# Performance work log

Hardware: AMD Instinct MI355X
Metric: run time of the kernel (lower is better)

Reference implementation:

```python
import jax, jax.numpy as jnp
import numpy as np

N = 100000      # nodes
E = 500000      # edges
NODE_IN = 60
EDGE_IN = 8
H = 256         # hidden
L = 8           # GINEConv layers
G = 64          # graphs in batch
BN_EPS = 1e-5


def setup_inputs() -> dict:
    key = jax.random.key(0)
    ks = jax.random.split(key, 40)
    s = 0.05
    f32 = jnp.float32
    inp = {
        "x": jax.random.normal(ks[0], (N, NODE_IN), f32),
        "edge_index": jax.random.randint(ks[1], (2, E), 0, N),
        "edge_attr": jax.random.normal(ks[2], (E, EDGE_IN), f32),
        "batch": jnp.sort(jax.random.randint(ks[3], (N,), 0, G)),
        # x_proj: Linear(node_in->H) + BatchNorm1d (eval-mode running stats)
        "xproj_W": jax.random.normal(ks[4], (NODE_IN, H), f32) * s,
        "xproj_b": jnp.zeros((H,), f32),
        "xp_gamma": jnp.ones((H,), f32),
        "xp_beta": jnp.zeros((H,), f32),
        "xp_mean": jax.random.normal(ks[5], (H,), f32) * 0.01,
        "xp_var": jax.random.uniform(ks[6], (H,), f32, 0.5, 1.5),
        # stacked GINEConv params (L layers)
        "edge_W": jax.random.normal(ks[7], (L, EDGE_IN, H), f32) * s,
        "edge_b": jnp.zeros((L, H), f32),
        "mlp_W1": jax.random.normal(ks[8], (L, H, H), f32) * s,
        "mlp_b1": jnp.zeros((L, H), f32),
        "mlp_W2": jax.random.normal(ks[9], (L, H, H), f32) * s,
        "mlp_b2": jnp.zeros((L, H), f32),
        "eps": jnp.zeros((L,), f32),  # GINE eps (default 0, not trained)
        # per-layer BatchNorm (eval-mode)
        "bn_gamma": jnp.ones((L, H), f32),
        "bn_beta": jnp.zeros((L, H), f32),
        "bn_mean": jax.random.normal(ks[10], (L, H), f32) * 0.01,
        "bn_var": jax.random.uniform(ks[11], (L, H), f32, 0.5, 1.5),
        # head: Linear(H->H/2) ReLU Dropout Linear(H/2->1)
        "head_W1": jax.random.normal(ks[12], (H, H // 2), f32) * s,
        "head_b1": jnp.zeros((H // 2,), f32),
        "head_W2": jax.random.normal(ks[13], (H // 2, 1), f32) * s,
        "head_b2": jnp.zeros((1,), f32),
    }
    return inp


def _bn(x, gamma, beta, mean, var):
    # eval-mode BatchNorm1d with running stats
    return (x - mean) * (gamma * jax.lax.rsqrt(var + BN_EPS)) + beta


def reference(x, edge_index, edge_attr, batch,
              xproj_W, xproj_b, xp_gamma, xp_beta, xp_mean, xp_var,
              edge_W, edge_b, mlp_W1, mlp_b1, mlp_W2, mlp_b2, eps,
              bn_gamma, bn_beta, bn_mean, bn_var,
              head_W1, head_b1, head_W2, head_b2):
    src, dst = edge_index[0], edge_index[1]  # source -> target aggregation
    # x_proj: Linear + BN + ReLU
    h = jax.nn.relu(_bn(x @ xproj_W + xproj_b, xp_gamma, xp_beta, xp_mean, xp_var))
    for l in range(L):
        # GINEConv: msg = ReLU(x_j + lin(edge_attr)); sum-aggregate at target
        e = edge_attr @ edge_W[l] + edge_b[l]                 # [E,H]
        m = jax.nn.relu(h[src] + e)                           # [E,H] gather + add
        agg = jax.ops.segment_sum(m, dst, num_segments=N)     # [N,H] scatter-add
        z = (1.0 + eps[l]) * h + agg
        z = jax.nn.relu(z @ mlp_W1[l] + mlp_b1[l]) @ mlp_W2[l] + mlp_b2[l]
        # BN + ReLU (dropout is identity in eval)
        h = jax.nn.relu(_bn(z, bn_gamma[l], bn_beta[l], bn_mean[l], bn_var[l]))
    # global_mean_pool over batch ids
    gsum = jax.ops.segment_sum(h, batch, num_segments=G)      # [G,H]
    cnt = jax.ops.segment_sum(jnp.ones((N, 1), h.dtype), batch, num_segments=G)
    g = gsum / jnp.maximum(cnt, 1.0)
    # head MLP -> scalar per graph
    hid = jax.nn.relu(g @ head_W1 + head_b1)
    out = (hid @ head_W2 + head_b2)[:, 0]                     # [G]
    return out
```

## Files before the change

kernel.cpp:

```cpp
#include <hip/hip_runtime.h>

#define N_NODES 100000
#define N_EDGES 500000
#define NODE_IN 60
#define EDGE_IN 8
#define HID 256
#define NLAYERS 8
#define NGRAPH 64
#define BN_EPS 1e-5f
#define SY_PITCH 520

typedef __attribute__((ext_vector_type(4))) float f32x4;
typedef __attribute__((ext_vector_type(4))) short short4v;
typedef __attribute__((ext_vector_type(8))) short short8v;
typedef __attribute__((ext_vector_type(4))) unsigned short u16x4;
typedef unsigned short u16;

__device__ __forceinline__ u16 f2bf(float f) {
    unsigned int u = __builtin_bit_cast(unsigned int, f);
    u += 0x7fffu + ((u >> 16) & 1u);
    return (u16)(u >> 16);
}
__device__ __forceinline__ float bf2f(u16 u) {
    unsigned int x = ((unsigned int)u) << 16;
    return __builtin_bit_cast(float, x);
}
__device__ __forceinline__ float lo_f(unsigned int d) {
    return __builtin_bit_cast(float, d << 16);
}
__device__ __forceinline__ float hi_f(unsigned int d) {
    return __builtin_bit_cast(float, d & 0xffff0000u);
}

__device__ __forceinline__ void g2lds16(const void* g, void* l) {
    __builtin_amdgcn_global_load_lds(
        (const __attribute__((address_space(1))) void*)g,
        (__attribute__((address_space(3))) void*)l, 16, 0, 0);
}

template<int KT, bool WITH_BN>
__global__ __launch_bounds__(256, 2)
void mfma_gemm(const u16* A, const u16* Bt,
               const float* __restrict__ bias,
               const float* __restrict__ gamma, const float* __restrict__ beta,
               const float* __restrict__ mean,  const float* __restrict__ var,
               u16* Cout, int M)
{
    __shared__ u16 smem[24576];
    u16* sA = smem;
    u16* sB = smem + 8192;

    const int tid  = threadIdx.x;
    const int lane = tid & 63;
    const int wv   = tid >> 6;
    const int lrow = lane & 15;
    const int g    = lane >> 4;
    const int m0   = blockIdx.x * 128;
    const int ldab = KT * 128;
    const int lsub = lane >> 3;
    const int gsw  = ((lane & 7) * 16) ^ (lsub << 4);

    f32x4 acc[8][4] = {};

    for (int kt = 0; kt < KT; ++kt) {
        #pragma unroll
        for (int i = 0; i < 4; ++i) {
            const int row = i * 32 + wv * 8 + lsub;
            g2lds16((const char*)A + (size_t)(m0 + row) * ldab + kt * 128 + gsw,
                    (char*)sA + i * 4096 + wv * 1024);
        }
        #pragma unroll
        for (int i = 0; i < 8; ++i) {
            const int row = i * 32 + wv * 8 + lsub;
            g2lds16((const char*)Bt + (size_t)row * ldab + kt * 128 + gsw,
                    (char*)sB + i * 4096 + wv * 1024);
        }
        __syncthreads();

        #pragma unroll
        for (int ks = 0; ks < 2; ++ks) {
            const int off1 = ks * 64 + 8 * g;
            const int off2 = off1 + 32;
            short8v bfrag[4];
            #pragma unroll
            for (int nb = 0; nb < 4; ++nb) {
                const int col = wv * 64 + nb * 16 + lrow;
                const int sw  = (col & 7) << 4;
                short4v lo = *(const short4v*)((const char*)sB + col * 128 + (off1 ^ sw));
                short4v hi = *(const short4v*)((const char*)sB + col * 128 + (off2 ^ sw));
                short8v b;
                b[0] = lo[0]; b[1] = lo[1]; b[2] = lo[2]; b[3] = lo[3];
                b[4] = hi[0]; b[5] = hi[1]; b[6] = hi[2]; b[7] = hi[3];
                bfrag[nb] = b;
            }
            #pragma unroll
            for (int mb = 0; mb < 8; ++mb) {
                const int row = mb * 16 + lrow;
                const int sw  = (row & 7) << 4;
                short4v lo = *(const short4v*)((const char*)sA + row * 128 + (off1 ^ sw));
                short4v hi = *(const short4v*)((const char*)sA + row * 128 + (off2 ^ sw));
                short8v a;
                a[0] = lo[0]; a[1] = lo[1]; a[2] = lo[2]; a[3] = lo[3];
                a[4] = hi[0]; a[5] = hi[1]; a[6] = hi[2]; a[7] = hi[3];
                #pragma unroll
                for (int nb = 0; nb < 4; ++nb)
                    acc[mb][nb] = __builtin_amdgcn_mfma_f32_16x16x32_bf16(a, bfrag[nb], acc[mb][nb], 0, 0, 0);
            }
        }
        __syncthreads();
    }

    #pragma unroll
    for (int mb = 0; mb < 8; ++mb) {
        #pragma unroll
        for (int r = 0; r < 4; ++r) {
            const int row = m0 + mb * 16 + g * 4 + r;
            if (row >= M) continue;
            #pragma unroll
            for (int nb = 0; nb < 4; ++nb) {
                const int col = wv * 64 + nb * 16 + lrow;
                float v = acc[mb][nb][r] + bias[col];
                if constexpr (WITH_BN)
                    v = (v - mean[col]) * (gamma[col] * rsqrtf(var[col] + BN_EPS)) + beta[col];
                v = fmaxf(v, 0.f);
                Cout[(size_t)row * HID + col] = f2bf(v);
            }
        }
    }
}

__global__ __launch_bounds__(256, 2)
void fused_mlp(const u16* __restrict__ Z, const u16* __restrict__ W1t,
               const u16* __restrict__ W2t,
               const float* __restrict__ b1,
               const float* __restrict__ scale2, const float* __restrict__ shift2,
               u16* __restrict__ Hout, int M)
{
    __shared__ u16 smem[37120];
    u16* sA = smem;
    u16* sB = sA + 4096;
    u16* sY = sB + 16384;

    const int tid  = threadIdx.x;
    const int lane = tid & 63;
    const int wv   = tid >> 6;
    const int lrow = lane & 15;
    const int g    = lane >> 4;
    const int m0   = blockIdx.x * 64;
    const int lsub = lane >> 3;
    const int gsw  = ((lane & 7) * 16) ^ (lsub << 4);

    f32x4 acc[4][4] = {};

    for (int kt = 0; kt < 4; ++kt) {
        #pragma unroll
        for (int i = 0; i < 2; ++i) {
            const int row = i * 32 + wv * 8 + lsub;
            g2lds16((const char*)Z + (size_t)(m0 + row) * 512 + kt * 128 + gsw,
                    (char*)sA + i * 4096 + wv * 1024);
        }
        #pragma unroll
        for (int i = 0; i < 8; ++i) {
            const int row = i * 32 + wv * 8 + lsub;
            g2lds16((const char*)W1t + (size_t)row * 512 + kt * 128 + gsw,
                    (char*)sB + i * 4096 + wv * 1024);
        }
        __syncthreads();

        #pragma unroll
        for (int ks = 0; ks < 2; ++ks) {
            const int off1 = ks * 64 + 8 * g;
            const int off2 = off1 + 32;
            short8v bfrag[4];
            #pragma unroll
            for (int nb = 0; nb < 4; ++nb) {
                const int col = wv * 64 + nb * 16 + lrow;
                const int sw  = (col & 7) << 4;
                short4v lo = *(const short4v*)((const char*)sB + col * 128 + (off1 ^ sw));
                short4v hi = *(const short4v*)((const char*)sB + col * 128 + (off2 ^ sw));
                short8v b;
                b[0] = lo[0]; b[1] = lo[1]; b[2] = lo[2]; b[3] = lo[3];
                b[4] = hi[0]; b[5] = hi[1]; b[6] = hi[2]; b[7] = hi[3];
                bfrag[nb] = b;
            }
            #pragma unroll
            for (int mb = 0; mb < 4; ++mb) {
                const int row = mb * 16 + lrow;
                const int sw  = (row & 7) << 4;
                short4v lo = *(const short4v*)((const char*)sA + row * 128 + (off1 ^ sw));
                short4v hi = *(const short4v*)((const char*)sA + row * 128 + (off2 ^ sw));
                short8v a;
                a[0] = lo[0]; a[1] = lo[1]; a[2] = lo[2]; a[3] = lo[3];
                a[4] = hi[0]; a[5] = hi[1]; a[6] = hi[2]; a[7] = hi[3];
                #pragma unroll
                for (int nb = 0; nb < 4; ++nb)
                    acc[mb][nb] = __builtin_amdgcn_mfma_f32_16x16x32_bf16(a, bfrag[nb], acc[mb][nb], 0, 0, 0);
            }
        }
        __syncthreads();
    }

    float b1v[4];
    #pragma unroll
    for (int nb = 0; nb < 4; ++nb) b1v[nb] = b1[wv * 64 + nb * 16 + lrow];
    #pragma unroll
    for (int mb = 0; mb < 4; ++mb) {
        #pragma unroll
        for (int r = 0; r < 4; ++r) {
            const int row = mb * 16 + g * 4 + r;
            #pragma unroll
            for (int nb = 0; nb < 4; ++nb) {
                const int col = wv * 64 + nb * 16 + lrow;
                const float v = fmaxf(acc[mb][nb][r] + b1v[nb], 0.f);
                *(u16*)((char*)sY + row * SY_PITCH + col * 2) = f2bf(v);
            }
        }
    }
    __syncthreads();

    f32x4 acc2[4][4] = {};
    for (int kt2 = 0; kt2 < 4; ++kt2) {
        #pragma unroll
        for (int i = 0; i < 8; ++i) {
            const int row = i * 32 + wv * 8 + lsub;
            g2lds16((const char*)W2t + (size_t)row * 512 + kt2 * 128 + gsw,
                    (char*)sB + i * 4096 + wv * 1024);
        }
        __syncthreads();

        #pragma unroll
        for (int ks = 0; ks < 2; ++ks) {
            const int off1 = ks * 64 + 8 * g;
            const int off2 = off1 + 32;
            const int yo1  = kt2 * 128 + off1;
            const int yo2  = yo1 + 32;
            short8v bfrag[4];
            #pragma unroll
            for (int nb = 0; nb < 4; ++nb) {
                const int col = wv * 64 + nb * 16 + lrow;
                const int sw  = (col & 7) << 4;
                short4v lo = *(const short4v*)((const char*)sB + col * 128 + (off1 ^ sw));
                short4v hi = *(const short4v*)((const char*)sB + col * 128 + (off2 ^ sw));
                short8v b;
                b[0] = lo[0]; b[1] = lo[1]; b[2] = lo[2]; b[3] = lo[3];
                b[4] = hi[0]; b[5] = hi[1]; b[6] = hi[2]; b[7] = hi[3];
                bfrag[nb] = b;
            }
            #pragma unroll
            for (int mb = 0; mb < 4; ++mb) {
                const int row = mb * 16 + lrow;
                short4v lo = *(const short4v*)((const char*)sY + row * SY_PITCH + yo1);
                short4v hi = *(const short4v*)((const char*)sY + row * SY_PITCH + yo2);
                short8v a;
                a[0] = lo[0]; a[1] = lo[1]; a[2] = lo[2]; a[3] = lo[3];
                a[4] = hi[0]; a[5] = hi[1]; a[6] = hi[2]; a[7] = hi[3];
                #pragma unroll
                for (int nb = 0; nb < 4; ++nb)
                    acc2[mb][nb] = __builtin_amdgcn_mfma_f32_16x16x32_bf16(a, bfrag[nb], acc2[mb][nb], 0, 0, 0);
            }
        }
        __syncthreads();
    }

    float scl[4], shf[4];
    #pragma unroll
    for (int nb = 0; nb < 4; ++nb) {
        const int col = wv * 64 + nb * 16 + lrow;
        scl[nb] = scale2[col];
        shf[nb] = shift2[col];
    }
    #pragma unroll
    for (int mb = 0; mb < 4; ++mb) {
        #pragma unroll
        for (int r = 0; r < 4; ++r) {
            const int row = m0 + mb * 16 + g * 4 + r;
            if (row >= M) continue;
            #pragma unroll
            for (int nb = 0; nb < 4; ++nb) {
                const int col = wv * 64 + nb * 16 + lrow;
                const float v = fmaxf(acc2[mb][nb][r] * scl[nb] + shf[nb], 0.f);
                Hout[(size_t)row * HID + col] = f2bf(v);
            }
        }
    }
}

__global__ __launch_bounds__(256)
void convw_kernel(const float* __restrict__ W, u16* __restrict__ Wt)
{
    size_t i = (size_t)blockIdx.x * 256 + threadIdx.x;
    const int mat = (int)(i >> 16);
    const int idx = (int)(i & 65535);
    const int n = idx >> 8, k = idx & 255;
    Wt[i] = f2bf(W[(size_t)mat * 65536 + (size_t)k * 256 + n]);
}

__global__ __launch_bounds__(256)
void convwx_kernel(const float* __restrict__ W, u16* __restrict__ Wt)
{
    int i = blockIdx.x * 256 + threadIdx.x;
    const int n = i >> 6, k = i & 63;
    Wt[i] = (k < NODE_IN) ? f2bf(W[(size_t)k * HID + n]) : (u16)0;
}

__global__ __launch_bounds__(256)
void convx_kernel(const float* __restrict__ x, u16* __restrict__ xbf)
{
    size_t i = (size_t)blockIdx.x * 256 + threadIdx.x;
    if (i >= (size_t)N_NODES * 64) return;
    const int n = (int)(i >> 6), k = (int)(i & 63);
    xbf[i] = (k < NODE_IN) ? f2bf(x[(size_t)n * NODE_IN + k]) : (u16)0;
}

__global__ __launch_bounds__(256)
void bnfold_kernel(const float* __restrict__ b2, const float* __restrict__ gamma,
                   const float* __restrict__ beta, const float* __restrict__ mean,
                   const float* __restrict__ var,
                   float* __restrict__ scale, float* __restrict__ shift)
{
    int i = blockIdx.x * 256 + threadIdx.x;
    if (i >= NLAYERS * HID) return;
    const float s = gamma[i] * rsqrtf(var[i] + BN_EPS);
    scale[i] = s;
    shift[i] = (b2[i] - mean[i]) * s + beta[i];
}

__global__ __launch_bounds__(256)
void deg_count_kernel(const int* __restrict__ dst, int* __restrict__ deg, int E)
{
    int e = blockIdx.x * 256 + threadIdx.x;
    if (e < E) atomicAdd(&deg[dst[e]], 1);
}

__global__ __launch_bounds__(256)
void scan1_kernel(const int* __restrict__ deg, int* __restrict__ rowptr,
                  int* __restrict__ bsum, int n)
{
    __shared__ int s[256];
    const int tid = threadIdx.x;
    const int i = blockIdx.x * 256 + tid;
    const int v = (i < n) ? deg[i] : 0;
    s[tid] = v;
    __syncthreads();
    #pragma unroll
    for (int d = 1; d < 256; d <<= 1) {
        int t = (tid >= d) ? s[tid - d] : 0;
        __syncthreads();
        s[tid] += t;
        __syncthreads();
    }
    if (i < n) rowptr[i] = s[tid] - v;
    if (tid == 255) bsum[blockIdx.x] = s[255];
}

__global__ void scan2_kernel(int* bsum, int nb, int* rowptr, int n)
{
    if (threadIdx.x == 0 && blockIdx.x == 0) {
        int run = 0;
        for (int j = 0; j < nb; ++j) { int t = bsum[j]; bsum[j] = run; run += t; }
        rowptr[n] = run;
    }
}

__global__ __launch_bounds__(256)
void scan3_kernel(int* __restrict__ rowptr, const int* __restrict__ bsum, int n)
{
    int i = blockIdx.x * 256 + threadIdx.x;
    if (i < n) rowptr[i] += bsum[i >> 8];
}

__global__ __launch_bounds__(256)
void scatter_kernel(const int* __restrict__ src, const int* __restrict__ dst,
                    const float* __restrict__ ea,
                    const int* __restrict__ rowptr, int* __restrict__ fill,
                    int* __restrict__ esrc, u16* __restrict__ eap, int E)
{
    int e = blockIdx.x * 256 + threadIdx.x;
    if (e >= E) return;
    const int d = dst[e];
    const int pos = rowptr[d] + atomicAdd(&fill[d], 1);
    esrc[pos] = src[e];
    const float4 a0 = *(const float4*)&ea[(size_t)e * EDGE_IN];
    const float4 a1 = *(const float4*)&ea[(size_t)e * EDGE_IN + 4];
    u16x4 p0, p1;
    p0[0] = f2bf(a0.x); p0[1] = f2bf(a0.y); p0[2] = f2bf(a0.z); p0[3] = f2bf(a0.w);
    p1[0] = f2bf(a1.x); p1[1] = f2bf(a1.y); p1[2] = f2bf(a1.z); p1[3] = f2bf(a1.w);
    *(u16x4*)&eap[(size_t)pos * EDGE_IN]     = p0;
    *(u16x4*)&eap[(size_t)pos * EDGE_IN + 4] = p1;
}

__global__ __launch_bounds__(256)
void agg_kernel(const u16* __restrict__ h, const u16* __restrict__ eap,
                const int* __restrict__ rowptr, const int* __restrict__ esrc,
                const float* __restrict__ W, const float* __restrict__ b,
                const float* __restrict__ eps, int l, u16* __restrict__ z)
{
    const int lane  = threadIdx.x & 63;
    const int wv    = threadIdx.x >> 6;
    const int c0    = lane * 4;
    const int lofsB = lane * 8;

    f32x4 Wr[EDGE_IN];
    #pragma unroll
    for (int k = 0; k < EDGE_IN; ++k) Wr[k] = *(const f32x4*)&W[k * HID + c0];
    const f32x4 br = *(const f32x4*)&b[c0];
    const float e1 = 1.0f + eps[l];

    for (int n = blockIdx.x * 4 + wv; n < N_NODES; n += gridDim.x * 4) {
        const int beg = __builtin_amdgcn_readfirstlane(rowptr[n]);
        const int end = __builtin_amdgcn_readfirstlane(rowptr[n + 1]);
        const int end1 = end - 1;

        const u16x4 hv = *(const u16x4*)&h[(size_t)n * HID + c0];
        float a0 = e1 * bf2f(hv[0]), a1 = e1 * bf2f(hv[1]);
        float a2 = e1 * bf2f(hv[2]), a3 = e1 * bf2f(hv[3]);

        for (int i0 = beg; i0 < end; i0 += 4) {
            int idx0 = i0;
            int idx1 = (i0 + 1 < end) ? i0 + 1 : end1;
            int idx2 = (i0 + 2 < end) ? i0 + 2 : end1;
            int idx3 = (i0 + 3 < end) ? i0 + 3 : end1;

            const int sb0 = __builtin_amdgcn_readfirstlane(esrc[idx0]) << 9;
            const int sb1 = __builtin_amdgcn_readfirstlane(esrc[idx1]) << 9;
            const int sb2 = __builtin_amdgcn_readfirstlane(esrc[idx2]) << 9;
            const int sb3 = __builtin_amdgcn_readfirstlane(esrc[idx3]) << 9;

            u16x4 hs0 = *(const u16x4*)((const char*)h + (unsigned)(sb0 + lofsB));
            u16x4 hs1 = *(const u16x4*)((const char*)h + (unsigned)(sb1 + lofsB));
            u16x4 hs2 = *(const u16x4*)((const char*)h + (unsigned)(sb2 + lofsB));
            u16x4 hs3 = *(const u16x4*)((const char*)h + (unsigned)(sb3 + lofsB));

            uint4 t0 = *(const uint4*)&eap[(size_t)idx0 * EDGE_IN];
            uint4 t1 = *(const uint4*)&eap[(size_t)idx1 * EDGE_IN];
            uint4 t2 = *(const uint4*)&eap[(size_t)idx2 * EDGE_IN];
            uint4 t3 = *(const uint4*)&eap[(size_t)idx3 * EDGE_IN];

            #pragma unroll
            for (int j = 0; j < 4; ++j) {
                if (i0 + j < end) {
                    const uint4 tt = (j == 0) ? t0 : (j == 1) ? t1 : (j == 2) ? t2 : t3;
                    const u16x4 hh = (j == 0) ? hs0 : (j == 1) ? hs1 : (j == 2) ? hs2 : hs3;
                    const unsigned dx = __builtin_amdgcn_readfirstlane((int)tt.x);
                    const unsigned dy = __builtin_amdgcn_readfirstlane((int)tt.y);
                    const unsigned dz = __builtin_amdgcn_readfirstlane((int)tt.z);
                    const unsigned dw = __builtin_amdgcn_readfirstlane((int)tt.w);
                    f32x4 ev = br;
                    ev += lo_f(dx) * Wr[0];
                    ev += hi_f(dx) * Wr[1];
                    ev += lo_f(dy) * Wr[2];
                    ev += hi_f(dy) * Wr[3];
                    ev += lo_f(dz) * Wr[4];
                    ev += hi_f(dz) * Wr[5];
                    ev += lo_f(dw) * Wr[6];
                    ev += hi_f(dw) * Wr[7];
                    a0 += fmaxf(bf2f(hh[0]) + ev[0], 0.f);
                    a1 += fmaxf(bf2f(hh[1]) + ev[1], 0.f);
                    a2 += fmaxf(bf2f(hh[2]) + ev[2], 0.f);
                    a3 += fmaxf(bf2f(hh[3]) + ev[3], 0.f);
                }
            }
        }
        u16x4 o;
        o[0] = f2bf(a0); o[1] = f2bf(a1); o[2] = f2bf(a2); o[3] = f2bf(a3);
        *(u16x4*)&z[(size_t)n * HID + c0] = o;
    }
}

__global__ __launch_bounds__(256)
void pool_kernel(const u16* __restrict__ h, const int* __restrict__ batch,
                 float* __restrict__ gsum, int* __restrict__ cnt, int n)
{
    const int lane = threadIdx.x & 63;
    const int wv   = threadIdx.x >> 6;
    const int c0   = lane * 4;
    const int n0   = blockIdx.x * 64;

    f32x4 acc = {0.f, 0.f, 0.f, 0.f};
    int gcur = -1;
    int c = 0;

    for (int i = wv; i < 64; i += 4) {
        const int node = n0 + i;
        if (node >= n) break;
        const int g = __builtin_amdgcn_readfirstlane(batch[node]);
        if (g != gcur) {
            if (gcur >= 0) {
                atomicAdd(&gsum[gcur * HID + c0 + 0], acc[0]);
                atomicAdd(&gsum[gcur * HID + c0 + 1], acc[1]);
                atomicAdd(&gsum[gcur * HID + c0 + 2], acc[2]);
                atomicAdd(&gsum[gcur * HID + c0 + 3], acc[3]);
                if (lane == 0) atomicAdd(&cnt[gcur], c);
            }
            acc = (f32x4){0.f, 0.f, 0.f, 0.f};
            c = 0;
            gcur = g;
        }
        const u16x4 hv = *(const u16x4*)&h[(size_t)node * HID + c0];
        acc[0] += bf2f(hv[0]);
        acc[1] += bf2f(hv[1]);
        acc[2] += bf2f(hv[2]);
        acc[3] += bf2f(hv[3]);
        c++;
    }
    if (gcur >= 0) {
        atomicAdd(&gsum[gcur * HID + c0 + 0], acc[0]);
        atomicAdd(&gsum[gcur * HID + c0 + 1], acc[1]);
        atomicAdd(&gsum[gcur * HID + c0 + 2], acc[2]);
        atomicAdd(&gsum[gcur * HID + c0 + 3], acc[3]);
        if (lane == 0) atomicAdd(&cnt[gcur], c);
    }
}

__global__ __launch_bounds__(128)
void head_kernel(const float* __restrict__ gsum, const int* __restrict__ cnt,
                 const float* __restrict__ W1, const float* __restrict__ b1,
                 const float* __restrict__ W2, const float* __restrict__ b2,
                 float* __restrict__ out)
{
    const int gi = blockIdx.x;
    const int j = threadIdx.x;
    __shared__ float gs[HID];
    __shared__ float red[128];

    const float c = fmaxf((float)cnt[gi], 1.0f);
    gs[j]       = gsum[gi * HID + j] / c;
    gs[j + 128] = gsum[gi * HID + 128 + j] / c;
    __syncthreads();

    float acc = b1[j];
    #pragma unroll 8
    for (int k = 0; k < HID; ++k) acc += gs[k] * W1[k * 128 + j];
    acc = fmaxf(acc, 0.f);
    red[j] = acc * W2[j];
    __syncthreads();
    for (int s = 64; s > 0; s >>= 1) {
        if (j < s) red[j] += red[j + s];
        __syncthreads();
    }
    if (j == 0) out[gi] = red[0] + b2[0];
}

extern "C" void kernel_launch(void* const* d_in, const int* in_sizes, int n_in,
                              void* d_out, int out_size, void* d_ws, size_t ws_size,
                              hipStream_t stream)
{
    const float* x         = (const float*)d_in[0];
    const int*   ei        = (const int*)d_in[1];
    const float* edge_attr = (const float*)d_in[2];
    const int*   batch     = (const int*)d_in[3];
    const float* xproj_W   = (const float*)d_in[4];
    const float* xproj_b   = (const float*)d_in[5];
    const float* xp_gamma  = (const float*)d_in[6];
    const float* xp_beta   = (const float*)d_in[7];
    const float* xp_mean   = (const float*)d_in[8];
    const float* xp_var    = (const float*)d_in[9];
    const float* edge_W    = (const float*)d_in[10];
    const float* edge_b    = (const float*)d_in[11];
    const float* mlp_W1    = (const float*)d_in[12];
    const float* mlp_b1    = (const float*)d_in[13];
    const float* mlp_W2    = (const float*)d_in[14];
    const float* mlp_b2    = (const float*)d_in[15];
    const float* eps       = (const float*)d_in[16];
    const float* bn_gamma  = (const float*)d_in[17];
    const float* bn_beta   = (const float*)d_in[18];
    const float* bn_mean   = (const float*)d_in[19];
    const float* bn_var    = (const float*)d_in[20];
    const float* head_W1   = (const float*)d_in[21];
    const float* head_b1   = (const float*)d_in[22];
    const float* head_W2   = (const float*)d_in[23];
    const float* head_b2   = (const float*)d_in[24];
    float* out = (float*)d_out;

    const int* srcI = ei;
    const int* dstI = ei + N_EDGES;

    char* w = (char*)d_ws;
    u16*   h      = (u16*)w;                 w += (size_t)N_NODES * HID * 2;
    u16*   zy     = (u16*)w;                 w += (size_t)N_NODES * HID * 2;
    u16*   xbf    = (u16*)w;                 w += (size_t)N_NODES * 64 * 2;
    u16*   Wt1    = (u16*)w;                 w += (size_t)NLAYERS * 65536 * 2;
    u16*   Wt2    = (u16*)w;                 w += (size_t)NLAYERS * 65536 * 2;
    u16*   Wxt    = (u16*)w;                 w += 16384 * 2;
    float* scale2 = (float*)w;               w += NLAYERS * HID * 4;
    float* shift2 = (float*)w;               w += NLAYERS * HID * 4;
    int*   rowptr = (int*)w;                 w += 100032 * 4;
    int*   deg    = (int*)w;                 w += 100032 * 4;
    int*   fill   = (int*)w;                 w += 100032 * 4;
    int*   bsum   = (int*)w;                 w += 512 * 4;
    int*   esrc   = (int*)w;                 w += (size_t)N_EDGES * 4;
    u16*   eap    = (u16*)w;                 w += (size_t)N_EDGES * EDGE_IN * 2;
    float* gsum   = (float*)w;               w += NGRAPH * HID * 4;
    int*   cnt    = (int*)w;                 w += NGRAPH * 4;

    convw_kernel<<<2048, 256, 0, stream>>>(mlp_W1, Wt1);
    convw_kernel<<<2048, 256, 0, stream>>>(mlp_W2, Wt2);
    convwx_kernel<<<64, 256, 0, stream>>>(xproj_W, Wxt);
    convx_kernel<<<25000, 256, 0, stream>>>(x, xbf);
    bnfold_kernel<<<8, 256, 0, stream>>>(mlp_b2, bn_gamma, bn_beta, bn_mean, bn_var,
                                         scale2, shift2);

    hipMemsetAsync(deg, 0, 2 * 100032 * sizeof(int), stream);
    deg_count_kernel<<<(N_EDGES + 255) / 256, 256, 0, stream>>>(dstI, deg, N_EDGES);
    scan1_kernel<<<391, 256, 0, stream>>>(deg, rowptr, bsum, N_NODES);
    scan2_kernel<<<1, 64, 0, stream>>>(bsum, 391, rowptr, N_NODES);
    scan3_kernel<<<391, 256, 0, stream>>>(rowptr, bsum, N_NODES);
    scatter_kernel<<<(N_EDGES + 255) / 256, 256, 0, stream>>>(
        srcI, dstI, edge_attr, rowptr, fill, esrc, eap, N_EDGES);

    mfma_gemm<1, true><<<(N_NODES + 127) / 128, 256, 0, stream>>>(
        xbf, Wxt, xproj_b, xp_gamma, xp_beta, xp_mean, xp_var, h, N_NODES);

    const int fgrid = (N_NODES + 63) / 64;
    for (int l = 0; l < NLAYERS; ++l) {
        agg_kernel<<<2048, 256, 0, stream>>>(
            h, eap, rowptr, esrc,
            edge_W + (size_t)l * EDGE_IN * HID, edge_b + (size_t)l * HID,
            eps, l, zy);
        fused_mlp<<<fgrid, 256, 0, stream>>>(
            zy, Wt1 + (size_t)l * 65536, Wt2 + (size_t)l * 65536,
            mlp_b1 + (size_t)l * HID, scale2 + (size_t)l * HID, shift2 + (size_t)l * HID,
            h, N_NODES);
    }

    hipMemsetAsync(gsum, 0, (NGRAPH * HID + NGRAPH) * sizeof(float), stream);
    pool_kernel<<<(N_NODES + 63) / 64, 256, 0, stream>>>(h, batch, gsum, cnt, N_NODES);
    head_kernel<<<NGRAPH, 128, 0, stream>>>(gsum, cnt, head_W1, head_b1, head_W2, head_b2, out);
}
```

Baseline: 1.128 ms.

## Split fused MLP into persistent GEMMs with LDS-resident weights

After: 1.284 ms. 1.14x slower.

```diff
diff --git a/kernel.cpp b/kernel.cpp
--- a/kernel.cpp
+++ b/kernel.cpp
@@ -8,7 +8,7 @@
 #define NLAYERS 8
 #define NGRAPH 64
 #define BN_EPS 1e-5f
-#define SY_PITCH 520
+#define NTILES (N_NODES / 32)
 
 typedef __attribute__((ext_vector_type(4))) float f32x4;
 typedef __attribute__((ext_vector_type(4))) short short4v;
@@ -129,157 +129,104 @@
     }
 }
 
-__global__ __launch_bounds__(256, 2)
-void fused_mlp(const u16* __restrict__ Z, const u16* __restrict__ W1t,
-               const u16* __restrict__ W2t,
-               const float* __restrict__ b1,
-               const float* __restrict__ scale2, const float* __restrict__ shift2,
-               u16* __restrict__ Hout, int M)
-{
-    __shared__ u16 smem[37120];
-    u16* sA = smem;
-    u16* sB = sA + 4096;
-    u16* sY = sB + 16384;
+template<bool WITH_BN>
+__global__ __launch_bounds__(512, 1)
+void pgemm(const u16* __restrict__ A, const u16* __restrict__ Wt,
+           const float* __restrict__ p0, const float* __restrict__ p1,
+           u16* __restrict__ Out, int M)
+{
+    __shared__ u16 smem[73728];
+    u16* sW = smem;
+    u16* sZ = smem + 65536;
 
     const int tid  = threadIdx.x;
     const int lane = tid & 63;
-    const int wv   = tid >> 6;
+    const int w    = tid >> 6;
     const int lrow = lane & 15;
     const int g    = lane >> 4;
-    const int m0   = blockIdx.x * 64;
-    const int lsub = lane >> 3;
-    const int gsw  = ((lane & 7) * 16) ^ (lsub << 4);
-
-    f32x4 acc[4][4] = {};
-
-    for (int kt = 0; kt < 4; ++kt) {
+
+    #pragma unroll
+    for (int i = 0; i < 16; ++i) {
+        const int seg = i * 512 + tid;
+        const int kt  = seg >> 11;
+        const int s2  = seg & 2047;
+        const int col = s2 >> 3;
+        const int j   = s2 & 7;
+        g2lds16((const char*)Wt + (size_t)col * 512 + kt * 128 + ((j * 16) ^ ((col & 7) << 4)),
+                (char*)sW + i * 8192 + w * 1024);
+    }
+
+    float e0[2], e1[2];
+    #pragma unroll
+    for (int nb = 0; nb < 2; ++nb) {
+        const int col = w * 32 + nb * 16 + lrow;
+        e0[nb] = p0[col];
+        e1[nb] = WITH_BN ? p1[col] : 0.f;
+    }
+
+    for (int t = blockIdx.x; t < NTILES; t += gridDim.x) {
+        const int m0 = t * 32;
+        __syncthreads();
         #pragma unroll
         for (int i = 0; i < 2; ++i) {
-            const int row = i * 32 + wv * 8 + lsub;
-            g2lds16((const char*)Z + (size_t)(m0 + row) * 512 + kt * 128 + gsw,
-                    (char*)sA + i * 4096 + wv * 1024);
-        }
-        #pragma unroll
-        for (int i = 0; i < 8; ++i) {
-            const int row = i * 32 + wv * 8 + lsub;
-            g2lds16((const char*)W1t + (size_t)row * 512 + kt * 128 + gsw,
-                    (char*)sB + i * 4096 + wv * 1024);
-        }
-        __syncthreads();
-
-        #pragma unroll
-        for (int ks = 0; ks < 2; ++ks) {
-            const int off1 = ks * 64 + 8 * g;
-            const int off2 = off1 + 32;
-            short8v bfrag[4];
+            const int seg = i * 512 + tid;
+            const int kt  = seg >> 8;
+            const int s2  = seg & 255;
+            const int row = s2 >> 3;
+            const int j   = s2 & 7;
+            g2lds16((const char*)A + (size_t)(m0 + row) * 512 + kt * 128 + ((j * 16) ^ ((row & 7) << 4)),
+                    (char*)sZ + i * 8192 + w * 1024);
+        }
+        __syncthreads();
+
+        f32x4 acc[2][2] = {};
+        #pragma unroll
+        for (int kt = 0; kt < 4; ++kt) {
             #pragma unroll
-            for (int nb = 0; nb < 4; ++nb) {
-                const int col = wv * 64 + nb * 16 + lrow;
-                const int sw  = (col & 7) << 4;
-                short4v lo = *(const short4v*)((const char*)sB + col * 128 + (off1 ^ sw));
-                short4v hi = *(const short4v*)((const char*)sB + col * 128 + (off2 ^ sw));
-                short8v b;
-                b[0] = lo[0]; b[1] = lo[1]; b[2] = lo[2]; b[3] = lo[3];
-                b[4] = hi[0]; b[5] = hi[1]; b[6] = hi[2]; b[7] = hi[3];
-                bfrag[nb] = b;
-            }
+            for (int ks = 0; ks < 2; ++ks) {
+                const int off1 = ks * 64 + 8 * g;
+                const int off2 = off1 + 32;
+                short8v bfrag[2];
+                #pragma unroll
+                for (int nb = 0; nb < 2; ++nb) {
+                    const int col = w * 32 + nb * 16 + lrow;
+                    const int sw  = (col & 7) << 4;
+                    short4v lo = *(const short4v*)((const char*)sW + kt * 32768 + col * 128 + (off1 ^ sw));
+                    short4v hi = *(const short4v*)((const char*)sW + kt * 32768 + col * 128 + (off2 ^ sw));
+                    short8v b;
+                    b[0] = lo[0]; b[1] = lo[1]; b[2] = lo[2]; b[3] = lo[3];
+                    b[4] = hi[0]; b[5] = hi[1]; b[6] = hi[2]; b[7] = hi[3];
+                    bfrag[nb] = b;
+                }
+                #pragma unroll
+                for (int mb = 0; mb < 2; ++mb) {
+                    const int row = mb * 16 + lrow;
+                    const int sw  = (row & 7) << 4;
+                    short4v lo = *(const short4v*)((const char*)sZ + kt * 4096 + row * 128 + (off1 ^ sw));
+                    short4v hi = *(const short4v*)((const char*)sZ + kt * 4096 + row * 128 + (off2 ^ sw));
+                    short8v a;
+                    a[0] = lo[0]; a[1] = lo[1]; a[2] = lo[2]; a[3] = lo[3];
+                    a[4] = hi[0]; a[5] = hi[1]; a[6] = hi[2]; a[7] = hi[3];
+                    #pragma unroll
+                    for (int nb = 0; nb < 2; ++nb)
+                        acc[mb][nb] = __builtin_amdgcn_mfma_f32_16x16x32_bf16(a, bfrag[nb], acc[mb][nb], 0, 0, 0);
+                }
+            }
+        }
+
+        #pragma unroll
+        for (int mb = 0; mb < 2; ++mb) {
             #pragma unroll
-            for (int mb = 0; mb < 4; ++mb) {
-                const int row = mb * 16 + lrow;
-                const int sw  = (row & 7) << 4;
-                short4v lo = *(const short4v*)((const char*)sA + row * 128 + (off1 ^ sw));
-                short4v hi = *(const short4v*)((const char*)sA + row * 128 + (off2 ^ sw));
-                short8v a;
-                a[0] = lo[0]; a[1] = lo[1]; a[2] = lo[2]; a[3] = lo[3];
-                a[4] = hi[0]; a[5] = hi[1]; a[6] = hi[2]; a[7] = hi[3];
+            for (int r = 0; r < 4; ++r) {
+                const int row = m0 + mb * 16 + g * 4 + r;
                 #pragma unroll
-                for (int nb = 0; nb < 4; ++nb)
-                    acc[mb][nb] = __builtin_amdgcn_mfma_f32_16x16x32_bf16(a, bfrag[nb], acc[mb][nb], 0, 0, 0);
-            }
-        }
-        __syncthreads();
-    }
-
-    float b1v[4];
-    #pragma unroll
-    for (int nb = 0; nb < 4; ++nb) b1v[nb] = b1[wv * 64 + nb * 16 + lrow];
-    #pragma unroll
-    for (int mb = 0; mb < 4; ++mb) {
-        #pragma unroll
-        for (int r = 0; r < 4; ++r) {
-            const int row = mb * 16 + g * 4 + r;
-            #pragma unroll
-            for (int nb = 0; nb < 4; ++nb) {
-                const int col = wv * 64 + nb * 16 + lrow;
-                const float v = fmaxf(acc[mb][nb][r] + b1v[nb], 0.f);
-                *(u16*)((char*)sY + row * SY_PITCH + col * 2) = f2bf(v);
-            }
-        }
-    }
-    __syncthreads();
-
-    f32x4 acc2[4][4] = {};
-    for (int kt2 = 0; kt2 < 4; ++kt2) {
-        #pragma unroll
-        for (int i = 0; i < 8; ++i) {
-            const int row = i * 32 + wv * 8 + lsub;
-            g2lds16((const char*)W2t + (size_t)row * 512 + kt2 * 128 + gsw,
-                    (char*)sB + i * 4096 + wv * 1024);
-        }
-        __syncthreads();
-
-        #pragma unroll
-        for (int ks = 0; ks < 2; ++ks) {
-            const int off1 = ks * 64 + 8 * g;
-            const int off2 = off1 + 32;
-            const int yo1  = kt2 * 128 + off1;
-            const int yo2  = yo1 + 32;
-            short8v bfrag[4];
-            #pragma unroll
-            for (int nb = 0; nb < 4; ++nb) {
-                const int col = wv * 64 + nb * 16 + lrow;
-                const int sw  = (col & 7) << 4;
-                short4v lo = *(const short4v*)((const char*)sB + col * 128 + (off1 ^ sw));
-                short4v hi = *(const short4v*)((const char*)sB + col * 128 + (off2 ^ sw));
-                short8v b;
-                b[0] = lo[0]; b[1] = lo[1]; b[2] = lo[2]; b[3] = lo[3];
-                b[4] = hi[0]; b[5] = hi[1]; b[6] = hi[2]; b[7] = hi[3];
-                bfrag[nb] = b;
-            }
-            #pragma unroll
-            for (int mb = 0; mb < 4; ++mb) {
-                const int row = mb * 16 + lrow;
-                short4v lo = *(const short4v*)((const char*)sY + row * SY_PITCH + yo1);
-                short4v hi = *(const short4v*)((const char*)sY + row * SY_PITCH + yo2);
-                short8v a;
-                a[0] = lo[0]; a[1] = lo[1]; a[2] = lo[2]; a[3] = lo[3];
-                a[4] = hi[0]; a[5] = hi[1]; a[6] = hi[2]; a[7] = hi[3];
-                #pragma unroll
-                for (int nb = 0; nb < 4; ++nb)
-                    acc2[mb][nb] = __builtin_amdgcn_mfma_f32_16x16x32_bf16(a, bfrag[nb], acc2[mb][nb], 0, 0, 0);
-            }
-        }
-        __syncthreads();
-    }
-
-    float scl[4], shf[4];
-    #pragma unroll
-    for (int nb = 0; nb < 4; ++nb) {
-        const int col = wv * 64 + nb * 16 + lrow;
-        scl[nb] = scale2[col];
-        shf[nb] = shift2[col];
-    }
-    #pragma unroll
-    for (int mb = 0; mb < 4; ++mb) {
-        #pragma unroll
-        for (int r = 0; r < 4; ++r) {
-            const int row = m0 + mb * 16 + g * 4 + r;
-            if (row >= M) continue;
-            #pragma unroll
-            for (int nb = 0; nb < 4; ++nb) {
-                const int col = wv * 64 + nb * 16 + lrow;
-                const float v = fmaxf(acc2[mb][nb][r] * scl[nb] + shf[nb], 0.f);
-                Hout[(size_t)row * HID + col] = f2bf(v);
+                for (int nb = 0; nb < 2; ++nb) {
+                    const int col = w * 32 + nb * 16 + lrow;
+                    float v;
+                    if constexpr (WITH_BN) v = fmaxf(acc[mb][nb][r] * e0[nb] + e1[nb], 0.f);
+                    else                   v = fmaxf(acc[mb][nb][r] + e0[nb], 0.f);
+                    Out[(size_t)row * HID + col] = f2bf(v);
+                }
             }
         }
     }
@@ -611,15 +558,15 @@
     mfma_gemm<1, true><<<(N_NODES + 127) / 128, 256, 0, stream>>>(
         xbf, Wxt, xproj_b, xp_gamma, xp_beta, xp_mean, xp_var, h, N_NODES);
 
-    const int fgrid = (N_NODES + 63) / 64;
     for (int l = 0; l < NLAYERS; ++l) {
         agg_kernel<<<2048, 256, 0, stream>>>(
             h, eap, rowptr, esrc,
             edge_W + (size_t)l * EDGE_IN * HID, edge_b + (size_t)l * HID,
             eps, l, zy);
-        fused_mlp<<<fgrid, 256, 0, stream>>>(
-            zy, Wt1 + (size_t)l * 65536, Wt2 + (size_t)l * 65536,
-            mlp_b1 + (size_t)l * HID, scale2 + (size_t)l * HID, shift2 + (size_t)l * HID,
+        pgemm<false><<<256, 512, 0, stream>>>(
+            zy, Wt1 + (size_t)l * 65536, mlp_b1 + (size_t)l * HID, nullptr, zy, N_NODES);
+        pgemm<true><<<256, 512, 0, stream>>>(
+            zy, Wt2 + (size_t)l * 65536, scale2 + (size_t)l * HID, shift2 + (size_t)l * HID,
             h, N_NODES);
     }
 
```
